# Optimization experiments

Measured on AMD Instinct MI355X. Metric: run time of the kernel, lower is better.

Reference implementation:

```python
import jax, jax.numpy as jnp
import numpy as np

NUM_HEADS = 16
KEY_DIM = 64
EPS = 1e-6


def setup_inputs() -> dict:
    key = jax.random.key(0)
    k0, k1, k2, k3, k4 = jax.random.split(key, 5)
    B, S, E = 4, 4096, NUM_HEADS * KEY_DIM
    scale = 1.0 / np.sqrt(KEY_DIM)
    return {
        "query": jax.random.normal(k0, (B, S, E), dtype=jnp.float32),
        "Wq": jax.random.normal(k1, (NUM_HEADS, KEY_DIM, KEY_DIM), dtype=jnp.float32) * scale,
        "Wk": jax.random.normal(k2, (NUM_HEADS, KEY_DIM, KEY_DIM), dtype=jnp.float32) * scale,
        "Wv": jax.random.normal(k3, (NUM_HEADS, KEY_DIM, KEY_DIM), dtype=jnp.float32) * scale,
        "Wo": jax.random.normal(k4, (E, E), dtype=jnp.float32) * (1.0 / np.sqrt(E)),
    }


def reference(query, Wq, Wk, Wv, Wo):
    # Self-attention: key = value = query (per call() defaults).
    B, S, E = query.shape
    H, D = NUM_HEADS, KEY_DIM
    # split_heads: (B, S, E) -> (B, H, S, D)
    x = jnp.transpose(query.reshape(B, S, H, D), (0, 2, 1, 3))
    # Per-head linear projections (all heads batched in one einsum each).
    q = jnp.einsum("bhsd,hde->bhse", x, Wq)
    k = jnp.einsum("bhsd,hde->bhse", x, Wk)
    v = jnp.einsum("bhsd,hde->bhse", x, Wv)
    # Kernel feature map phi(x) = elu(x) + 1 (strictly positive).
    phi_q = jax.nn.elu(q) + 1.0
    phi_k = jax.nn.elu(k) + 1.0
    # Linear (non-causal) attention: O(S*D^2) instead of O(S^2*D).
    kv = jnp.einsum("bhsd,bhse->bhde", phi_k, v)        # (B,H,D,D)
    k_sum = jnp.sum(phi_k, axis=2)                       # (B,H,D)
    z = jnp.einsum("bhsd,bhd->bhs", phi_q, k_sum)        # (B,H,S)
    ctx = jnp.einsum("bhsd,bhde->bhse", phi_q, kv) / (z[..., None] + EPS)
    # combine_heads: (B,H,S,D) -> (B,S,E), then output projection (no bias).
    combined = jnp.transpose(ctx, (0, 2, 1, 3)).reshape(B, S, H * D)
    return combined @ Wo
```

## Files before the change

### kernel.cpp

```cpp
#include <hip/hip_runtime.h>
#include <stdint.h>

#define S_LEN 4096
#define NHEADS 16
#define DHEAD 64
#define EMB 1024
#define NBATCH 4
#define NBH (NBATCH * NHEADS)

typedef unsigned short u16t;
typedef __attribute__((ext_vector_type(8))) short short8;
typedef __attribute__((ext_vector_type(4))) float f32x4;

__device__ __forceinline__ u16t f2bf(float f) {
  unsigned int x = __float_as_uint(f);
  x += 0x7fffu + ((x >> 16) & 1u);
  return (u16t)(x >> 16);
}
__device__ __forceinline__ unsigned int pack2(float a, float b) {
  return (unsigned int)f2bf(a) | ((unsigned int)f2bf(b) << 16);
}
__device__ __forceinline__ float bf2f(u16t u) { return __uint_as_float(((unsigned int)u) << 16); }
__device__ __forceinline__ float phifn(float v) { return v > 0.f ? v + 1.f : __expf(v); }

__device__ __forceinline__ void stage_w8k(const u16t* __restrict__ wg,
                                          u16t* __restrict__ lds, int t) {
#pragma unroll
  for (int c = 0; c < 2; ++c) {
    const u16t* src = wg + (size_t)(c * 256 + t) * 8;
    char* dst = (char*)lds + c * 4096 + ((t >> 6) << 10);
    __builtin_amdgcn_global_load_lds((const __attribute__((address_space(1))) unsigned int*)src,
                                     (__attribute__((address_space(3))) unsigned int*)dst,
                                     16, 0, 0);
  }
}

__global__ __launch_bounds__(256) void la_prep(const float* __restrict__ Wq,
                                               const float* __restrict__ Wk,
                                               const float* __restrict__ Wv,
                                               u16t* __restrict__ WqT,
                                               u16t* __restrict__ WkT,
                                               u16t* __restrict__ WvT) {
  __shared__ float tmp[64][65];
  int blk = blockIdx.x;
  int mat = blk >> 4, h = blk & 15;
  const float* src = (mat == 0 ? Wq : (mat == 1 ? Wk : Wv)) + (size_t)h * 4096;
  u16t* dst = (mat == 0 ? WqT : (mat == 1 ? WkT : WvT)) + (size_t)h * 4096;
  int t = threadIdx.x;
#pragma unroll
  for (int p = 0; p < 16; ++p) {
    int i = p * 256 + t;
    tmp[i >> 6][i & 63] = src[i];
  }
  __syncthreads();
#pragma unroll
  for (int p = 0; p < 16; ++p) {
    int i = p * 256 + t;
    int e = i >> 6, r = i & 63, o = r >> 3, j = r & 7;
    dst[i] = f2bf(tmp[((o ^ (e & 7)) << 3) + j][e]);
  }
}

__global__ __launch_bounds__(256) void la_wot(const float* __restrict__ Wo,
                                              u16t* __restrict__ WoT) {
  __shared__ float t[64][65];
  int n0 = blockIdx.x * 64, k0 = blockIdx.y * 64;
  int tx = threadIdx.x, ty = threadIdx.y;
  for (int r = ty; r < 64; r += 4) t[r][tx] = Wo[(size_t)(k0 + r) * EMB + n0 + tx];
  __syncthreads();
  for (int r = ty; r < 64; r += 4)
    WoT[(size_t)(n0 + r) * EMB + k0 + tx] = f2bf(t[tx][r]);
}

__global__ __launch_bounds__(256) void la_kvq4(const float* __restrict__ q,
                                               const u16t* __restrict__ WqT,
                                               const u16t* __restrict__ WkT,
                                               const u16t* __restrict__ WvT,
                                               u16t* __restrict__ phiq,
                                               float* __restrict__ kvpart,
                                               float* __restrict__ kspart) {
  __shared__ u16t xs[128 * 72];
  __shared__ u16t wq[4096];
  __shared__ u16t wk[4096];
  __shared__ u16t wv[4096];
  __shared__ u16t pkT[64 * 136];
  __shared__ u16t vT[64 * 136];
  __shared__ float ksp4[4][64];
  int blk = blockIdx.x;
  int bh = blk >> 3, tile = blk & 7;
  int b = bh >> 4, h = bh & 15;
  int s0 = tile << 9;
  int t = threadIdx.x;
  int wave = t >> 6, lane = t & 63, l16 = lane & 15, g = lane >> 4;

  stage_w8k(WqT + (size_t)h * 4096, wq, t);
  stage_w8k(WkT + (size_t)h * 4096, wk, t);
  stage_w8k(WvT + (size_t)h * 4096, wv, t);

  const float* xg = q + ((size_t)b * S_LEN + s0) * EMB + h * 64;
  int pr_r = t >> 4, pr_c4 = (t & 15) * 4;

  float4 pre[8];
#pragma unroll
  for (int i = 0; i < 8; ++i)
    pre[i] = *(const float4*)(xg + (size_t)(i * 16 + pr_r) * EMB + pr_c4);

  f32x4 kacc[4];
#pragma unroll
  for (int n = 0; n < 4; ++n) kacc[n] = 0.f;
  float ks_acc = 0.f;
  int ks_e = t & 63, ks_q = t >> 6;

  for (int c = 0; c < 4; ++c) {
    if (c) __syncthreads();
#pragma unroll
    for (int i = 0; i < 8; ++i) {
      uint2 p;
      p.x = pack2(pre[i].x, pre[i].y);
      p.y = pack2(pre[i].z, pre[i].w);
      *(uint2*)(&xs[(i * 16 + pr_r) * 72 + pr_c4]) = p;
    }
    if (c < 3) {
#pragma unroll
      for (int i = 0; i < 8; ++i)
        pre[i] = *(const float4*)(xg + (size_t)((c + 1) * 128 + i * 16 + pr_r) * EMB + pr_c4);
    }
    __syncthreads();

    f32x4 aQ[2][4], aK[2][4], aV[2][4];
#pragma unroll
    for (int m = 0; m < 2; ++m)
#pragma unroll
      for (int n = 0; n < 4; ++n) { aQ[m][n] = 0.f; aK[m][n] = 0.f; aV[m][n] = 0.f; }
    short8 af[2][2];
#pragma unroll
    for (int m = 0; m < 2; ++m)
#pragma unroll
      for (int kk = 0; kk < 2; ++kk)
        af[m][kk] = *(const short8*)(&xs[(wave * 32 + m * 16 + l16) * 72 + kk * 32 + g * 8]);
#pragma unroll
    for (int n = 0; n < 4; ++n) {
      int e = n * 16 + l16;
#pragma unroll
      for (int kk = 0; kk < 2; ++kk) {
        int op = (kk * 4 + g) ^ (l16 & 7);
        short8 bQ = *(const short8*)(&wq[e * 64 + op * 8]);
        short8 bK = *(const short8*)(&wk[e * 64 + op * 8]);
        short8 bV = *(const short8*)(&wv[e * 64 + op * 8]);
#pragma unroll
        for (int m = 0; m < 2; ++m) {
          aQ[m][n] = __builtin_amdgcn_mfma_f32_16x16x32_bf16(af[m][kk], bQ, aQ[m][n], 0, 0, 0);
          aK[m][n] = __builtin_amdgcn_mfma_f32_16x16x32_bf16(af[m][kk], bK, aK[m][n], 0, 0, 0);
          aV[m][n] = __builtin_amdgcn_mfma_f32_16x16x32_bf16(af[m][kk], bV, aV[m][n], 0, 0, 0);
        }
      }
    }
    __syncthreads();

#pragma unroll
    for (int m = 0; m < 2; ++m)
#pragma unroll
      for (int n = 0; n < 4; ++n) {
        int e = n * 16 + l16;
        int sb = wave * 32 + m * 16 + g * 4;
        uint2 pk2, vv2;
        pk2.x = pack2(phifn(aK[m][n][0]), phifn(aK[m][n][1]));
        pk2.y = pack2(phifn(aK[m][n][2]), phifn(aK[m][n][3]));
        vv2.x = pack2(aV[m][n][0], aV[m][n][1]);
        vv2.y = pack2(aV[m][n][2], aV[m][n][3]);
        *(uint2*)(&pkT[e * 136 + sb]) = pk2;
        *(uint2*)(&vT[e * 136 + sb]) = vv2;
#pragma unroll
        for (int j = 0; j < 4; ++j) xs[(sb + j) * 72 + e] = f2bf(phifn(aQ[m][n][j]));
      }
    __syncthreads();

#pragma unroll
    for (int i = 0; i < 4; ++i) {
      int slot = i * 256 + t;
      int r = slot >> 3, cc = (slot & 7) * 8;
      *(uint4*)(phiq + ((size_t)bh * S_LEN + s0 + c * 128 + r) * 64 + cc) =
          *(const uint4*)(&xs[r * 72 + cc]);
    }
#pragma unroll
    for (int ks = 0; ks < 4; ++ks) {
      short8 pa = *(const short8*)(&pkT[(wave * 16 + l16) * 136 + ks * 32 + g * 8]);
#pragma unroll
      for (int n = 0; n < 4; ++n) {
        short8 vb = *(const short8*)(&vT[(n * 16 + l16) * 136 + ks * 32 + g * 8]);
        kacc[n] = __builtin_amdgcn_mfma_f32_16x16x32_bf16(pa, vb, kacc[n], 0, 0, 0);
      }
    }
#pragma unroll
    for (int i = 0; i < 8; ++i) {
      uint2 u = *(const uint2*)(&pkT[ks_e * 136 + ks_q * 32 + i * 4]);
      ks_acc += bf2f((u16t)(u.x & 0xffff)) + bf2f((u16t)(u.x >> 16)) +
                bf2f((u16t)(u.y & 0xffff)) + bf2f((u16t)(u.y >> 16));
    }
  }

  float* kp = kvpart + (size_t)blk * 4096;
#pragma unroll
  for (int n = 0; n < 4; ++n)
#pragma unroll
    for (int j = 0; j < 4; ++j)
      kp[(wave * 16 + g * 4 + j) * 64 + n * 16 + l16] = kacc[n][j];

  ksp4[ks_q][ks_e] = ks_acc;
  __syncthreads();
  if (t < 64)
    kspart[(size_t)blk * 64 + t] = ksp4[0][t] + ksp4[1][t] + ksp4[2][t] + ksp4[3][t];
}

__global__ __launch_bounds__(256) void la_red3(const float* __restrict__ kvpart,
                                               const float* __restrict__ kspart,
                                               const u16t* __restrict__ WoT,
                                               float* __restrict__ ksum_g,
                                               u16t* __restrict__ W2T) {
  __shared__ float kvs[64][65];
  __shared__ u16t aT[256 * 72];
  int bh = blockIdx.x;
  int b = bh >> 4, h = bh & 15;
  int t = threadIdx.x, wave = t >> 6, lane = t & 63, l16 = lane & 15, g = lane >> 4;

  float acc[16];
#pragma unroll
  for (int i = 0; i < 16; ++i) acc[i] = 0.f;
  for (int p = 0; p < 8; ++p) {
    const float* base = kvpart + ((size_t)bh * 8 + p) * 4096;
#pragma unroll
    for (int i = 0; i < 16; ++i) acc[i] += base[i * 256 + t];
  }
#pragma unroll
  for (int i = 0; i < 16; ++i) {
    int idx = i * 256 + t;
    kvs[idx >> 6][idx & 63] = acc[i];
  }
  if (t < 64) {
    float a = 0.f;
    for (int p = 0; p < 8; ++p) a += kspart[((size_t)bh * 8 + p) * 64 + t];
    ksum_g[(size_t)bh * 64 + t] = a;
  }
  __syncthreads();

  short8 kvbf[4][2];
#pragma unroll
  for (int n = 0; n < 4; ++n)
#pragma unroll
    for (int kk = 0; kk < 2; ++kk) {
      u16t* pp = (u16t*)&kvbf[n][kk];
#pragma unroll
      for (int i = 0; i < 8; ++i) pp[i] = f2bf(kvs[n * 16 + l16][kk * 32 + g * 8 + i]);
    }

  for (int ec = 0; ec < 4; ++ec) {
    if (ec) __syncthreads();
#pragma unroll
    for (int p = 0; p < 8; ++p) {
      int slot = p * 256 + t;
      int r = slot >> 3, cc = (slot & 7) * 8;
      *(uint4*)(&aT[r * 72 + cc]) =
          *(const uint4*)(WoT + (size_t)(ec * 256 + r) * 1024 + h * 64 + cc);
    }
    __syncthreads();
    f32x4 c2[4][4];
#pragma unroll
    for (int mi = 0; mi < 4; ++mi)
#pragma unroll
      for (int n = 0; n < 4; ++n) c2[mi][n] = 0.f;
#pragma unroll
    for (int kk = 0; kk < 2; ++kk)
#pragma unroll
      for (int mi = 0; mi < 4; ++mi) {
        short8 afr = *(const short8*)(&aT[(wave * 64 + mi * 16 + l16) * 72 + kk * 32 + g * 8]);
#pragma unroll
        for (int n = 0; n < 4; ++n)
          c2[mi][n] = __builtin_amdgcn_mfma_f32_16x16x32_bf16(afr, kvbf[n][kk], c2[mi][n], 0, 0, 0);
      }
    __syncthreads();
#pragma unroll
    for (int mi = 0; mi < 4; ++mi)
#pragma unroll
      for (int n = 0; n < 4; ++n)
#pragma unroll
        for (int j = 0; j < 4; ++j)
          aT[(wave * 64 + mi * 16 + g * 4 + j) * 72 + n * 16 + l16] = f2bf(c2[mi][n][j]);
    __syncthreads();
#pragma unroll
    for (int p = 0; p < 8; ++p) {
      int slot = p * 256 + t;
      int r = slot >> 3, cc = (slot & 7) * 8;
      *(uint4*)(W2T + ((size_t)b << 20) + (size_t)(ec * 256 + r) * 1024 + h * 64 + cc) =
          *(const uint4*)(&aT[r * 72 + cc]);
    }
  }
}

__global__ __launch_bounds__(256) void la_scale(const u16t* __restrict__ phiq,
                                                const float* __restrict__ ksum_g,
                                                u16t* __restrict__ phiq2) {
  __shared__ float ks[64];
  int blk = blockIdx.x;
  int bh = blk >> 4, sl = blk & 15;
  int b = bh >> 4, h = bh & 15;
  int s0 = sl * 256;
  int t = threadIdx.x;
  if (t < 64) ks[t] = ksum_g[(size_t)bh * 64 + t];
  __syncthreads();
  int c16 = t & 15, rg = t >> 4;
#pragma unroll 2
  for (int it = 0; it < 16; ++it) {
    int s = s0 + it * 16 + rg;
    uint2 u = *(const uint2*)(phiq + ((size_t)bh * S_LEN + s) * 64 + c16 * 4);
    float f0 = bf2f((u16t)(u.x & 0xffff)), f1 = bf2f((u16t)(u.x >> 16));
    float f2 = bf2f((u16t)(u.y & 0xffff)), f3 = bf2f((u16t)(u.y >> 16));
    float zp = f0 * ks[c16 * 4] + f1 * ks[c16 * 4 + 1] + f2 * ks[c16 * 4 + 2] + f3 * ks[c16 * 4 + 3];
    zp += __shfl_xor(zp, 1);
    zp += __shfl_xor(zp, 2);
    zp += __shfl_xor(zp, 4);
    zp += __shfl_xor(zp, 8);
    float inv = 1.f / (zp + 1e-6f);
    uint2 o;
    o.x = pack2(f0 * inv, f1 * inv);
    o.y = pack2(f2 * inv, f3 * inv);
    *(uint2*)(phiq2 + ((size_t)(b * S_LEN + s)) * EMB + h * 64 + c16 * 4) = o;
  }
}

__device__ __forceinline__ void stage_half(const u16t* __restrict__ gbase,
                                           u16t* __restrict__ lbuf,
                                           int half, int t) {
#pragma unroll
  for (int it = 0; it < 2; ++it) {
    int slot = it * 512 + t;
    int row = half * 128 + (slot >> 3);
    int oct = slot & 7;
    const u16t* src = gbase + (size_t)row * EMB + (((oct ^ (row & 7)) << 3));
    char* dst = (char*)lbuf + ((half * 128 + it * 64 + ((t >> 6) << 3)) << 7);
    __builtin_amdgcn_global_load_lds((const __attribute__((address_space(1))) unsigned int*)src,
                                     (__attribute__((address_space(3))) unsigned int*)dst,
                                     16, 0, 0);
  }
}

#define GFENCE asm volatile("" ::: "memory")

#define LOAD_A(QM)                                                              \
  _Pragma("unroll") for (int mi = 0; mi < 4; ++mi) _Pragma("unroll")            \
      for (int kk = 0; kk < 2; ++kk) {                                          \
    int rr = (QM) * 128 + wr2 * 64 + mi * 16 + l16;                             \
    afr[mi][kk] = *(const short8*)((const char*)Acur + rr * 128 +               \
                                   ((((kk << 2) | g) ^ (rr & 7)) << 4));        \
  }
#define LOAD_B(QN, DST)                                                         \
  _Pragma("unroll") for (int ni = 0; ni < 2; ++ni) _Pragma("unroll")            \
      for (int kk = 0; kk < 2; ++kk) {                                          \
    int rr = (QN) * 128 + wc2 * 32 + ni * 16 + l16;                             \
    DST[ni][kk] = *(const short8*)((const char*)Bcur + rr * 128 +               \
                                   ((((kk << 2) | g) ^ (rr & 7)) << 4));        \
  }
#define MFMA_Q(QM, QN, BF)                                                      \
  __builtin_amdgcn_s_setprio(1);                                                \
  _Pragma("unroll") for (int mi = 0; mi < 4; ++mi) _Pragma("unroll")            \
      for (int ni = 0; ni < 2; ++ni) {                                          \
    acc[QM][QN][mi][ni] = __builtin_amdgcn_mfma_f32_16x16x32_bf16(              \
        afr[mi][0], BF[ni][0], acc[QM][QN][mi][ni], 0, 0, 0);                   \
    acc[QM][QN][mi][ni] = __builtin_amdgcn_mfma_f32_16x16x32_bf16(              \
        afr[mi][1], BF[ni][1], acc[QM][QN][mi][ni], 0, 0, 0);                   \
  }                                                                             \
  __builtin_amdgcn_s_setprio(0);

#define BAR()                      \
  __builtin_amdgcn_s_barrier();    \
  GFENCE

__global__ __launch_bounds__(512, 2) void la_gemm9(const u16t* __restrict__ A,
                                                   const u16t* __restrict__ W2T,
                                                   float* __restrict__ C) {
  __shared__ u16t Al[2][16384];
  __shared__ u16t Bl[2][16384];
  int t = threadIdx.x;
  int bid = blockIdx.x;
  int swz = ((bid & 7) << 5) + (bid >> 3);
  int mt = swz >> 2, nt = swz & 3;
  const int M0 = mt * 256, N0 = nt * 256;
  const int b = mt >> 4;
  int wave = t >> 6, lane = t & 63;
  int l16 = lane & 15, g = lane >> 4;
  int wr2 = wave >> 2, wc2 = wave & 3;

  f32x4 acc[2][2][4][2];
#pragma unroll
  for (int qm = 0; qm < 2; ++qm)
#pragma unroll
    for (int qn = 0; qn < 2; ++qn)
#pragma unroll
      for (int mi = 0; mi < 4; ++mi)
#pragma unroll
        for (int ni = 0; ni < 2; ++ni) acc[qm][qn][mi][ni] = 0.f;

  const u16t* Asrc = A + (size_t)M0 * EMB;
  const u16t* Bsrc = W2T + ((size_t)b << 20) + (size_t)N0 * EMB;

  stage_half(Asrc, Al[0], 0, t);
  stage_half(Bsrc, Bl[0], 0, t);
  stage_half(Bsrc, Bl[0], 1, t);
  stage_half(Asrc, Al[0], 1, t);
  asm volatile("s_waitcnt vmcnt(4)" ::: "memory");
  BAR();

  short8 afr[4][2], bf0[2][2], bf1[2][2];

  for (int kt = 0; kt < 15; ++kt) {
    const u16t* Acur = Al[kt & 1];
    const u16t* Bcur = Bl[kt & 1];
    u16t* Anxt = Al[(kt + 1) & 1];
    u16t* Bnxt = Bl[(kt + 1) & 1];
    const u16t* An = Asrc + (kt + 1) * 64;
    const u16t* Bn = Bsrc + (kt + 1) * 64;
    LOAD_A(0);
    LOAD_B(0, bf0);
    stage_half(An, Anxt, 0, t);
    stage_half(Bn, Bnxt, 0, t);
    asm volatile("s_waitcnt vmcnt(6)" ::: "memory");
    BAR();
    MFMA_Q(0, 0, bf0);
    GFENCE;
    BAR();
    LOAD_B(1, bf1);
    stage_half(Bn, Bnxt, 1, t);
    asm volatile("s_waitcnt vmcnt(6)" ::: "memory");
    BAR();
    MFMA_Q(0, 1, bf1);
    GFENCE;
    BAR();
    LOAD_A(1);
    stage_half(An, Anxt, 1, t);
    BAR();
    MFMA_Q(1, 1, bf1);
    GFENCE;
    BAR();
    asm volatile("s_waitcnt vmcnt(4)" ::: "memory");
    BAR();
    MFMA_Q(1, 0, bf0);
    GFENCE;
    BAR();
  }
  {
    const u16t* Acur = Al[1];
    const u16t* Bcur = Bl[1];
    LOAD_A(0);
    LOAD_B(0, bf0);
    asm volatile("s_waitcnt vmcnt(2)" ::: "memory");
    BAR();
    MFMA_Q(0, 0, bf0);
    GFENCE;
    BAR();
    LOAD_B(1, bf1);
    asm volatile("s_waitcnt vmcnt(0)" ::: "memory");
    BAR();
    MFMA_Q(0, 1, bf1);
    GFENCE;
    BAR();
    LOAD_A(1);
    BAR();
    MFMA_Q(1, 1, bf1);
    GFENCE;
    BAR();
    BAR();
    MFMA_Q(1, 0, bf0);
    GFENCE;
  }

#pragma unroll
  for (int qm = 0; qm < 2; ++qm)
#pragma unroll
    for (int qn = 0; qn < 2; ++qn)
#pragma unroll
      for (int mi = 0; mi < 4; ++mi)
#pragma unroll
        for (int ni = 0; ni < 2; ++ni)
#pragma unroll
          for (int j = 0; j < 4; ++j) {
            int row = M0 + qm * 128 + wr2 * 64 + mi * 16 + g * 4 + j;
            int col = N0 + qn * 128 + wc2 * 32 + ni * 16 + l16;
            C[(size_t)row * EMB + col] = acc[qm][qn][mi][ni][j];
          }
}

extern "C" void kernel_launch(void* const* d_in, const int* in_sizes, int n_in,
                              void* d_out, int out_size, void* d_ws, size_t ws_size,
                              hipStream_t stream) {
  const float* query = (const float*)d_in[0];
  const float* Wq = (const float*)d_in[1];
  const float* Wk = (const float*)d_in[2];
  const float* Wv = (const float*)d_in[3];
  const float* Wo = (const float*)d_in[4];
  float* out = (float*)d_out;
  char* ws = (char*)d_ws;

  u16t* WoT     = (u16t*)(ws);
  u16t* WqT     = (u16t*)(ws + 2097152);
  u16t* WkT     = (u16t*)(ws + 2228224);
  u16t* WvT     = (u16t*)(ws + 2359296);
  u16t* phiq    = (u16t*)(ws + 2490368);
  float* kvpart = (float*)(ws + 36044800);
  float* kspart = (float*)(ws + 44433408);
  float* ksum_g = (float*)(ws + 44564480);
  u16t* W2T     = (u16t*)(ws + 44580864);
  u16t* phiq2   = (u16t*)(ws + 52969472);

  la_prep<<<48, 256, 0, stream>>>(Wq, Wk, Wv, WqT, WkT, WvT);
  la_wot<<<dim3(16, 16), dim3(64, 4), 0, stream>>>(Wo, WoT);
  la_kvq4<<<512, 256, 0, stream>>>(query, WqT, WkT, WvT, phiq, kvpart, kspart);
  la_red3<<<NBH, 256, 0, stream>>>(kvpart, kspart, WoT, ksum_g, W2T);
  la_scale<<<1024, 256, 0, stream>>>(phiq, ksum_g, phiq2);
  la_gemm9<<<256, 512, 0, stream>>>(phiq2, W2T, out);
}
```

Baseline: 112.1 us.

## Replace 256x256 eight-wave GEMM with simpler 128x128 four-wave double-buffered GEMM

Rewrites the final output-projection GEMM to use 128x128 tiles with 256-thread blocks and 1024 blocks, replacing the 256x256 tile, 512-thread kernel and its quadrant-interleaved load/MFMA schedule. Each k-step now issues the next tile's global-to-LDS loads, waits, then runs all 32 MFMAs per wave in one block. The aim is more blocks to fill all CUs and lower LDS use per block, for better occupancy and less barrier overhead. In exchange it lowers operand reuse per tile, raising global and LDS traffic, and drops the fine-grained overlap of the old schedule.

Result: slower. 119.8 us (+6.8%).

```diff
diff --git a/kernel.cpp b/kernel.cpp
--- a/kernel.cpp
+++ b/kernel.cpp
@@ -327,16 +327,15 @@
   }
 }
 
-__device__ __forceinline__ void stage_half(const u16t* __restrict__ gbase,
-                                           u16t* __restrict__ lbuf,
-                                           int half, int t) {
-#pragma unroll
-  for (int it = 0; it < 2; ++it) {
-    int slot = it * 512 + t;
-    int row = half * 128 + (slot >> 3);
-    int oct = slot & 7;
-    const u16t* src = gbase + (size_t)row * EMB + (((oct ^ (row & 7)) << 3));
-    char* dst = (char*)lbuf + ((half * 128 + it * 64 + ((t >> 6) << 3)) << 7);
+__device__ __forceinline__ void stage_tile(const u16t* __restrict__ gbase,
+                                           u16t* __restrict__ lds, int t) {
+#pragma unroll
+  for (int it = 0; it < 4; ++it) {
+    int slot = it * 256 + t;
+    int row = slot >> 3, oct = slot & 7;
+    int octd = oct ^ (row & 7);
+    const u16t* src = gbase + (size_t)row * 1024 + octd * 8;
+    char* dst = (char*)lds + it * 4096 + ((t >> 6) << 10);
     __builtin_amdgcn_global_load_lds((const __attribute__((address_space(1))) unsigned int*)src,
                                      (__attribute__((address_space(3))) unsigned int*)dst,
                                      16, 0, 0);
@@ -344,148 +343,83 @@
 }
 
 #define GFENCE asm volatile("" ::: "memory")
-
-#define LOAD_A(QM)                                                              \
-  _Pragma("unroll") for (int mi = 0; mi < 4; ++mi) _Pragma("unroll")            \
-      for (int kk = 0; kk < 2; ++kk) {                                          \
-    int rr = (QM) * 128 + wr2 * 64 + mi * 16 + l16;                             \
-    afr[mi][kk] = *(const short8*)((const char*)Acur + rr * 128 +               \
-                                   ((((kk << 2) | g) ^ (rr & 7)) << 4));        \
-  }
-#define LOAD_B(QN, DST)                                                         \
-  _Pragma("unroll") for (int ni = 0; ni < 2; ++ni) _Pragma("unroll")            \
-      for (int kk = 0; kk < 2; ++kk) {                                          \
-    int rr = (QN) * 128 + wc2 * 32 + ni * 16 + l16;                             \
-    DST[ni][kk] = *(const short8*)((const char*)Bcur + rr * 128 +               \
-                                   ((((kk << 2) | g) ^ (rr & 7)) << 4));        \
-  }
-#define MFMA_Q(QM, QN, BF)                                                      \
-  __builtin_amdgcn_s_setprio(1);                                                \
-  _Pragma("unroll") for (int mi = 0; mi < 4; ++mi) _Pragma("unroll")            \
-      for (int ni = 0; ni < 2; ++ni) {                                          \
-    acc[QM][QN][mi][ni] = __builtin_amdgcn_mfma_f32_16x16x32_bf16(              \
-        afr[mi][0], BF[ni][0], acc[QM][QN][mi][ni], 0, 0, 0);                   \
-    acc[QM][QN][mi][ni] = __builtin_amdgcn_mfma_f32_16x16x32_bf16(              \
-        afr[mi][1], BF[ni][1], acc[QM][QN][mi][ni], 0, 0, 0);                   \
-  }                                                                             \
-  __builtin_amdgcn_s_setprio(0);
-
 #define BAR()                      \
   __builtin_amdgcn_s_barrier();    \
   GFENCE
 
-__global__ __launch_bounds__(512, 2) void la_gemm9(const u16t* __restrict__ A,
-                                                   const u16t* __restrict__ W2T,
-                                                   float* __restrict__ C) {
-  __shared__ u16t Al[2][16384];
-  __shared__ u16t Bl[2][16384];
+__global__ __launch_bounds__(256) void la_gemm11(const u16t* __restrict__ A,
+                                                 const u16t* __restrict__ W2T,
+                                                 float* __restrict__ C) {
+  __shared__ u16t Al[2][8192];
+  __shared__ u16t Bl[2][8192];
   int t = threadIdx.x;
   int bid = blockIdx.x;
-  int swz = ((bid & 7) << 5) + (bid >> 3);
-  int mt = swz >> 2, nt = swz & 3;
-  const int M0 = mt * 256, N0 = nt * 256;
-  const int b = mt >> 4;
+  int swz = ((bid & 7) << 7) + (bid >> 3);
+  int mt = swz >> 3, nt = swz & 7;
+  const int M0 = mt * 128, N0 = nt * 128;
+  const int b = mt >> 5;
   int wave = t >> 6, lane = t & 63;
   int l16 = lane & 15, g = lane >> 4;
-  int wr2 = wave >> 2, wc2 = wave & 3;
-
-  f32x4 acc[2][2][4][2];
-#pragma unroll
-  for (int qm = 0; qm < 2; ++qm)
-#pragma unroll
-    for (int qn = 0; qn < 2; ++qn)
-#pragma unroll
-      for (int mi = 0; mi < 4; ++mi)
-#pragma unroll
-        for (int ni = 0; ni < 2; ++ni) acc[qm][qn][mi][ni] = 0.f;
+  int wr = wave >> 1, wc = wave & 1;
+
+  f32x4 acc[4][4];
+#pragma unroll
+  for (int m = 0; m < 4; ++m)
+#pragma unroll
+    for (int n = 0; n < 4; ++n) acc[m][n] = 0.f;
 
   const u16t* Asrc = A + (size_t)M0 * EMB;
   const u16t* Bsrc = W2T + ((size_t)b << 20) + (size_t)N0 * EMB;
 
-  stage_half(Asrc, Al[0], 0, t);
-  stage_half(Bsrc, Bl[0], 0, t);
-  stage_half(Bsrc, Bl[0], 1, t);
-  stage_half(Asrc, Al[0], 1, t);
-  asm volatile("s_waitcnt vmcnt(4)" ::: "memory");
-  BAR();
-
-  short8 afr[4][2], bf0[2][2], bf1[2][2];
-
-  for (int kt = 0; kt < 15; ++kt) {
-    const u16t* Acur = Al[kt & 1];
-    const u16t* Bcur = Bl[kt & 1];
-    u16t* Anxt = Al[(kt + 1) & 1];
-    u16t* Bnxt = Bl[(kt + 1) & 1];
-    const u16t* An = Asrc + (kt + 1) * 64;
-    const u16t* Bn = Bsrc + (kt + 1) * 64;
-    LOAD_A(0);
-    LOAD_B(0, bf0);
-    stage_half(An, Anxt, 0, t);
-    stage_half(Bn, Bnxt, 0, t);
-    asm volatile("s_waitcnt vmcnt(6)" ::: "memory");
+  stage_tile(Asrc, &Al[0][0], t);
+  stage_tile(Bsrc, &Bl[0][0], t);
+
+  for (int kt = 0; kt < 16; ++kt) {
+    const u16t* Acur = &Al[kt & 1][0];
+    const u16t* Bcur = &Bl[kt & 1][0];
+    if (kt < 15) {
+      stage_tile(Asrc + (kt + 1) * 64, &Al[(kt + 1) & 1][0], t);
+      stage_tile(Bsrc + (kt + 1) * 64, &Bl[(kt + 1) & 1][0], t);
+      asm volatile("s_waitcnt vmcnt(8)" ::: "memory");
+    } else {
+      asm volatile("s_waitcnt vmcnt(0)" ::: "memory");
+    }
     BAR();
-    MFMA_Q(0, 0, bf0);
+    short8 af[4][2], bf[4][2];
+#pragma unroll
+    for (int m = 0; m < 4; ++m)
+#pragma unroll
+      for (int kk = 0; kk < 2; ++kk) {
+        int row = wr * 64 + m * 16 + l16;
+        af[m][kk] = *(const short8*)((const char*)Acur + row * 128 +
+                                     ((((kk << 2) | g) ^ (row & 7)) << 4));
+        int col = wc * 64 + m * 16 + l16;
+        bf[m][kk] = *(const short8*)((const char*)Bcur + col * 128 +
+                                     ((((kk << 2) | g) ^ (col & 7)) << 4));
+      }
+    __builtin_amdgcn_s_setprio(1);
+#pragma unroll
+    for (int m = 0; m < 4; ++m)
+#pragma unroll
+      for (int n = 0; n < 4; ++n) {
+        acc[m][n] = __builtin_amdgcn_mfma_f32_16x16x32_bf16(af[m][0], bf[n][0], acc[m][n], 0, 0, 0);
+        acc[m][n] = __builtin_amdgcn_mfma_f32_16x16x32_bf16(af[m][1], bf[n][1], acc[m][n], 0, 0, 0);
+      }
+    __builtin_amdgcn_s_setprio(0);
     GFENCE;
-    BAR();
-    LOAD_B(1, bf1);
-    stage_half(Bn, Bnxt, 1, t);
-    asm volatile("s_waitcnt vmcnt(6)" ::: "memory");
-    BAR();
-    MFMA_Q(0, 1, bf1);
-    GFENCE;
-    BAR();
-    LOAD_A(1);
-    stage_half(An, Anxt, 1, t);
-    BAR();
-    MFMA_Q(1, 1, bf1);
-    GFENCE;
-    BAR();
-    asm volatile("s_waitcnt vmcnt(4)" ::: "memory");
-    BAR();
-    MFMA_Q(1, 0, bf0);
-    GFENCE;
-    BAR();
-  }
-  {
-    const u16t* Acur = Al[1];
-    const u16t* Bcur = Bl[1];
-    LOAD_A(0);
-    LOAD_B(0, bf0);
-    asm volatile("s_waitcnt vmcnt(2)" ::: "memory");
-    BAR();
-    MFMA_Q(0, 0, bf0);
-    GFENCE;
-    BAR();
-    LOAD_B(1, bf1);
-    asm volatile("s_waitcnt vmcnt(0)" ::: "memory");
-    BAR();
-    MFMA_Q(0, 1, bf1);
-    GFENCE;
-    BAR();
-    LOAD_A(1);
-    BAR();
-    MFMA_Q(1, 1, bf1);
-    GFENCE;
-    BAR();
-    BAR();
-    MFMA_Q(1, 0, bf0);
-    GFENCE;
-  }
-
-#pragma unroll
-  for (int qm = 0; qm < 2; ++qm)
-#pragma unroll
-    for (int qn = 0; qn < 2; ++qn)
-#pragma unroll
-      for (int mi = 0; mi < 4; ++mi)
-#pragma unroll
-        for (int ni = 0; ni < 2; ++ni)
-#pragma unroll
-          for (int j = 0; j < 4; ++j) {
-            int row = M0 + qm * 128 + wr2 * 64 + mi * 16 + g * 4 + j;
-            int col = N0 + qn * 128 + wc2 * 32 + ni * 16 + l16;
-            C[(size_t)row * EMB + col] = acc[qm][qn][mi][ni][j];
-          }
+    if (kt < 15) BAR();
+  }
+
+#pragma unroll
+  for (int m = 0; m < 4; ++m)
+#pragma unroll
+    for (int n = 0; n < 4; ++n)
+#pragma unroll
+      for (int j = 0; j < 4; ++j) {
+        int row = M0 + wr * 64 + m * 16 + g * 4 + j;
+        int col = N0 + wc * 64 + n * 16 + l16;
+        C[(size_t)row * EMB + col] = acc[m][n][j];
+      }
 }
 
 extern "C" void kernel_launch(void* const* d_in, const int* in_sizes, int n_in,
@@ -515,5 +449,5 @@
   la_kvq4<<<512, 256, 0, stream>>>(query, WqT, WkT, WvT, phiq, kvpart, kspart);
   la_red3<<<NBH, 256, 0, stream>>>(kvpart, kspart, WoT, ksum_g, W2T);
   la_scale<<<1024, 256, 0, stream>>>(phiq, ksum_g, phiq2);
-  la_gemm9<<<256, 512, 0, stream>>>(phiq2, W2T, out);
-}
+  la_gemm11<<<1024, 256, 0, stream>>>(phiq2, W2T, out);
+}
```

## Recompute Q projection in scale kernel instead of storing phi(q) intermediate

Applied to the files above, without the earlier changes.

Moves the Q projection and phi feature map out of the KV kernel and into the normalization kernel, which now reads the fp32 input, projects with Wq, applies phi, computes z against k_sum and writes the scaled bf16 phi(q) directly. This removes the bf16 phi(q) write and re-read through global memory. In exchange the fp32 query tensor is read twice (once in the KV pass, once in the new kernel), and the new kernel does extra MFMA work per tile with more blocks.

After: 112.7 us. About the same (+0.5%).

```diff
diff --git a/kernel.cpp b/kernel.cpp
--- a/kernel.cpp
+++ b/kernel.cpp
@@ -72,15 +72,12 @@
     WoT[(size_t)(n0 + r) * EMB + k0 + tx] = f2bf(t[tx][r]);
 }
 
-__global__ __launch_bounds__(256) void la_kvq4(const float* __restrict__ q,
-                                               const u16t* __restrict__ WqT,
-                                               const u16t* __restrict__ WkT,
-                                               const u16t* __restrict__ WvT,
-                                               u16t* __restrict__ phiq,
-                                               float* __restrict__ kvpart,
-                                               float* __restrict__ kspart) {
+__global__ __launch_bounds__(256) void la_kv(const float* __restrict__ q,
+                                             const u16t* __restrict__ WkT,
+                                             const u16t* __restrict__ WvT,
+                                             float* __restrict__ kvpart,
+                                             float* __restrict__ kspart) {
   __shared__ u16t xs[128 * 72];
-  __shared__ u16t wq[4096];
   __shared__ u16t wk[4096];
   __shared__ u16t wv[4096];
   __shared__ u16t pkT[64 * 136];
@@ -93,7 +90,6 @@
   int t = threadIdx.x;
   int wave = t >> 6, lane = t & 63, l16 = lane & 15, g = lane >> 4;
 
-  stage_w8k(WqT + (size_t)h * 4096, wq, t);
   stage_w8k(WkT + (size_t)h * 4096, wk, t);
   stage_w8k(WvT + (size_t)h * 4096, wv, t);
 
@@ -127,11 +123,11 @@
     }
     __syncthreads();
 
-    f32x4 aQ[2][4], aK[2][4], aV[2][4];
+    f32x4 aK[2][4], aV[2][4];
 #pragma unroll
     for (int m = 0; m < 2; ++m)
 #pragma unroll
-      for (int n = 0; n < 4; ++n) { aQ[m][n] = 0.f; aK[m][n] = 0.f; aV[m][n] = 0.f; }
+      for (int n = 0; n < 4; ++n) { aK[m][n] = 0.f; aV[m][n] = 0.f; }
     short8 af[2][2];
 #pragma unroll
     for (int m = 0; m < 2; ++m)
@@ -144,19 +140,15 @@
 #pragma unroll
       for (int kk = 0; kk < 2; ++kk) {
         int op = (kk * 4 + g) ^ (l16 & 7);
-        short8 bQ = *(const short8*)(&wq[e * 64 + op * 8]);
         short8 bK = *(const short8*)(&wk[e * 64 + op * 8]);
         short8 bV = *(const short8*)(&wv[e * 64 + op * 8]);
 #pragma unroll
         for (int m = 0; m < 2; ++m) {
-          aQ[m][n] = __builtin_amdgcn_mfma_f32_16x16x32_bf16(af[m][kk], bQ, aQ[m][n], 0, 0, 0);
           aK[m][n] = __builtin_amdgcn_mfma_f32_16x16x32_bf16(af[m][kk], bK, aK[m][n], 0, 0, 0);
           aV[m][n] = __builtin_amdgcn_mfma_f32_16x16x32_bf16(af[m][kk], bV, aV[m][n], 0, 0, 0);
         }
       }
     }
-    __syncthreads();
-
 #pragma unroll
     for (int m = 0; m < 2; ++m)
 #pragma unroll
@@ -170,18 +162,9 @@
         vv2.y = pack2(aV[m][n][2], aV[m][n][3]);
         *(uint2*)(&pkT[e * 136 + sb]) = pk2;
         *(uint2*)(&vT[e * 136 + sb]) = vv2;
-#pragma unroll
-        for (int j = 0; j < 4; ++j) xs[(sb + j) * 72 + e] = f2bf(phifn(aQ[m][n][j]));
       }
     __syncthreads();
 
-#pragma unroll
-    for (int i = 0; i < 4; ++i) {
-      int slot = i * 256 + t;
-      int r = slot >> 3, cc = (slot & 7) * 8;
-      *(uint4*)(phiq + ((size_t)bh * S_LEN + s0 + c * 128 + r) * 64 + cc) =
-          *(const uint4*)(&xs[r * 72 + cc]);
-    }
 #pragma unroll
     for (int ks = 0; ks < 4; ++ks) {
       short8 pa = *(const short8*)(&pkT[(wave * 16 + l16) * 136 + ks * 32 + g * 8]);
@@ -296,34 +279,101 @@
   }
 }
 
-__global__ __launch_bounds__(256) void la_scale(const u16t* __restrict__ phiq,
-                                                const float* __restrict__ ksum_g,
-                                                u16t* __restrict__ phiq2) {
+__global__ __launch_bounds__(256) void la_qscale(const float* __restrict__ q,
+                                                 const u16t* __restrict__ WqT,
+                                                 const float* __restrict__ ksum_g,
+                                                 u16t* __restrict__ phiq2) {
+  __shared__ u16t xs[128 * 72];
+  __shared__ u16t wq[4096];
   __shared__ float ks[64];
   int blk = blockIdx.x;
-  int bh = blk >> 4, sl = blk & 15;
+  int bh = blk >> 5, tile = blk & 31;
   int b = bh >> 4, h = bh & 15;
-  int s0 = sl * 256;
+  int s0 = tile << 7;
   int t = threadIdx.x;
+  int wave = t >> 6, lane = t & 63, l16 = lane & 15, g = lane >> 4;
+
+  stage_w8k(WqT + (size_t)h * 4096, wq, t);
   if (t < 64) ks[t] = ksum_g[(size_t)bh * 64 + t];
-  __syncthreads();
-  int c16 = t & 15, rg = t >> 4;
-#pragma unroll 2
-  for (int it = 0; it < 16; ++it) {
-    int s = s0 + it * 16 + rg;
-    uint2 u = *(const uint2*)(phiq + ((size_t)bh * S_LEN + s) * 64 + c16 * 4);
-    float f0 = bf2f((u16t)(u.x & 0xffff)), f1 = bf2f((u16t)(u.x >> 16));
-    float f2 = bf2f((u16t)(u.y & 0xffff)), f3 = bf2f((u16t)(u.y >> 16));
-    float zp = f0 * ks[c16 * 4] + f1 * ks[c16 * 4 + 1] + f2 * ks[c16 * 4 + 2] + f3 * ks[c16 * 4 + 3];
-    zp += __shfl_xor(zp, 1);
-    zp += __shfl_xor(zp, 2);
-    zp += __shfl_xor(zp, 4);
-    zp += __shfl_xor(zp, 8);
-    float inv = 1.f / (zp + 1e-6f);
-    uint2 o;
-    o.x = pack2(f0 * inv, f1 * inv);
-    o.y = pack2(f2 * inv, f3 * inv);
-    *(uint2*)(phiq2 + ((size_t)(b * S_LEN + s)) * EMB + h * 64 + c16 * 4) = o;
+
+  const float* xg = q + ((size_t)b * S_LEN + s0) * EMB + h * 64;
+  int pr_r = t >> 4, pr_c4 = (t & 15) * 4;
+#pragma unroll
+  for (int i = 0; i < 8; ++i) {
+    float4 v = *(const float4*)(xg + (size_t)(i * 16 + pr_r) * EMB + pr_c4);
+    uint2 p;
+    p.x = pack2(v.x, v.y);
+    p.y = pack2(v.z, v.w);
+    *(uint2*)(&xs[(i * 16 + pr_r) * 72 + pr_c4]) = p;
+  }
+  __syncthreads();
+
+  f32x4 aQ[2][4];
+#pragma unroll
+  for (int m = 0; m < 2; ++m)
+#pragma unroll
+    for (int n = 0; n < 4; ++n) aQ[m][n] = 0.f;
+  short8 af[2][2];
+#pragma unroll
+  for (int m = 0; m < 2; ++m)
+#pragma unroll
+    for (int kk = 0; kk < 2; ++kk)
+      af[m][kk] = *(const short8*)(&xs[(wave * 32 + m * 16 + l16) * 72 + kk * 32 + g * 8]);
+#pragma unroll
+  for (int n = 0; n < 4; ++n) {
+    int e = n * 16 + l16;
+#pragma unroll
+    for (int kk = 0; kk < 2; ++kk) {
+      int op = (kk * 4 + g) ^ (l16 & 7);
+      short8 bQ = *(const short8*)(&wq[e * 64 + op * 8]);
+#pragma unroll
+      for (int m = 0; m < 2; ++m)
+        aQ[m][n] = __builtin_amdgcn_mfma_f32_16x16x32_bf16(af[m][kk], bQ, aQ[m][n], 0, 0, 0);
+    }
+  }
+
+  float ph[2][4][4];
+#pragma unroll
+  for (int m = 0; m < 2; ++m)
+#pragma unroll
+    for (int n = 0; n < 4; ++n)
+#pragma unroll
+      for (int j = 0; j < 4; ++j) ph[m][n][j] = phifn(aQ[m][n][j]);
+
+  float inv[2][4];
+#pragma unroll
+  for (int m = 0; m < 2; ++m)
+#pragma unroll
+    for (int j = 0; j < 4; ++j) {
+      float zp = 0.f;
+#pragma unroll
+      for (int n = 0; n < 4; ++n) zp = fmaf(ph[m][n][j], ks[n * 16 + l16], zp);
+      zp += __shfl_xor(zp, 1);
+      zp += __shfl_xor(zp, 2);
+      zp += __shfl_xor(zp, 4);
+      zp += __shfl_xor(zp, 8);
+      inv[m][j] = 1.f / (zp + 1e-6f);
+    }
+  __syncthreads();
+
+#pragma unroll
+  for (int m = 0; m < 2; ++m)
+#pragma unroll
+    for (int n = 0; n < 4; ++n) {
+      int e = n * 16 + l16;
+      int sb = wave * 32 + m * 16 + g * 4;
+#pragma unroll
+      for (int j = 0; j < 4; ++j)
+        xs[(sb + j) * 72 + e] = f2bf(ph[m][n][j] * inv[m][j]);
+    }
+  __syncthreads();
+
+#pragma unroll
+  for (int i = 0; i < 4; ++i) {
+    int slot = i * 256 + t;
+    int r = slot >> 3, cc = (slot & 7) * 8;
+    *(uint4*)(phiq2 + ((size_t)(b * S_LEN + s0 + r)) * EMB + h * 64 + cc) =
+        *(const uint4*)(&xs[r * 72 + cc]);
   }
 }
 
@@ -503,17 +553,16 @@
   u16t* WqT     = (u16t*)(ws + 2097152);
   u16t* WkT     = (u16t*)(ws + 2228224);
   u16t* WvT     = (u16t*)(ws + 2359296);
-  u16t* phiq    = (u16t*)(ws + 2490368);
-  float* kvpart = (float*)(ws + 36044800);
-  float* kspart = (float*)(ws + 44433408);
-  float* ksum_g = (float*)(ws + 44564480);
-  u16t* W2T     = (u16t*)(ws + 44580864);
-  u16t* phiq2   = (u16t*)(ws + 52969472);
+  float* kvpart = (float*)(ws + 2490368);
+  float* kspart = (float*)(ws + 10878976);
+  float* ksum_g = (float*)(ws + 11010048);
+  u16t* W2T     = (u16t*)(ws + 11026432);
+  u16t* phiq2   = (u16t*)(ws + 19415040);
 
   la_prep<<<48, 256, 0, stream>>>(Wq, Wk, Wv, WqT, WkT, WvT);
   la_wot<<<dim3(16, 16), dim3(64, 4), 0, stream>>>(Wo, WoT);
-  la_kvq4<<<512, 256, 0, stream>>>(query, WqT, WkT, WvT, phiq, kvpart, kspart);
+  la_kv<<<512, 256, 0, stream>>>(query, WkT, WvT, kvpart, kspart);
   la_red3<<<NBH, 256, 0, stream>>>(kvpart, kspart, WoT, ksum_g, W2T);
-  la_scale<<<1024, 256, 0, stream>>>(phiq, ksum_g, phiq2);
+  la_qscale<<<2048, 256, 0, stream>>>(query, WqT, ksum_g, phiq2);
   la_gemm9<<<256, 512, 0, stream>>>(phiq2, W2T, out);
 }
```
